# Kernel optimization log

Measured on AMD Instinct MI355X. Metric: run time of the kernel, lower is better.

The kernel has to match this reference:

```python
import jax, jax.numpy as jnp
import numpy as np

# (in_dim, out_dim) for fc1..fc14, hard-coded in the torch module
DIMS = [(12,12),(12,11),(11,10),(10,9),(9,8),(8,7),(7,6),(6,7),(7,8),(8,9),(9,10),(10,11),(11,12),(12,2)]
BATCH = 2_000_000


def setup_inputs() -> dict:
    key = jax.random.key(0)
    keys = jax.random.split(key, 2 * len(DIMS) + 1)
    inp = {"x": jax.random.normal(keys[0], (BATCH, 12), dtype=jnp.float32)}
    for i, (din, dout) in enumerate(DIMS):
        s = 1.0 / np.sqrt(din)  # torch nn.Linear default init range
        inp[f"w{i+1}"] = jax.random.uniform(keys[2*i+1], (dout, din), jnp.float32, -s, s)
        inp[f"b{i+1}"] = jax.random.uniform(keys[2*i+2], (dout,), jnp.float32, -s, s)
    return inp


def _forward(x, Ws, Bs):
    lin = lambda h, i: h @ Ws[i].T + Bs[i]
    # encoder half: fc1..fc6 with ReLU, saving identities 1..6
    ids = []
    h = x
    for i in range(6):
        h = jax.nn.relu(lin(h, i))
        ids.append(h)
    # bottleneck fc7
    h = jax.nn.relu(lin(h, 6))
    # decoder half: fc8..fc13, each adds the matching identity before ReLU
    # fc8 (+id6), fc9 (+id5), ..., fc13 (+id1)
    for i in range(7, 13):
        h = jax.nn.relu(lin(h, i) + ids[12 - i])
    # fc14 + softmax over class dim
    return jax.nn.softmax(lin(h, 13), axis=1)


def reference(x, w1, b1, w2, b2, w3, b3, w4, b4, w5, b5, w6, b6, w7, b7,
              w8, b8, w9, b9, w10, b10, w11, b11, w12, b12, w13, b13, w14, b14):
    Ws = [w1, w2, w3, w4, w5, w6, w7, w8, w9, w10, w11, w12, w13, w14]
    Bs = [b1, b2, b3, b4, b5, b6, b7, b8, b9, b10, b11, b12, b13, b14]
    return _forward(x, Ws, Bs)
```

## Files before the change

kernel.cpp:

```cpp
#include <hip/hip_runtime.h>
#include <math.h>

#define DEV __device__ __forceinline__

template <int DIN, int DOUT>
DEV void lin(const float* __restrict__ w, const float* __restrict__ b,
             const float* in, float* out) {
#pragma unroll
    for (int o = 0; o < DOUT; ++o) out[o] = b[o];
#pragma unroll
    for (int k = 0; k < DIN; ++k) {
        float xk = in[k];
#pragma unroll
        for (int o = 0; o < DOUT; ++o)
            out[o] = __builtin_fmaf(xk, w[o * DIN + k], out[o]);
    }
}

template <int DIN, int DOUT>
DEV void lin_skip(const float* __restrict__ w, const float* __restrict__ b,
                  const float* in, const float* skip, float* out) {
#pragma unroll
    for (int o = 0; o < DOUT; ++o) out[o] = b[o] + skip[o];
#pragma unroll
    for (int k = 0; k < DIN; ++k) {
        float xk = in[k];
#pragma unroll
        for (int o = 0; o < DOUT; ++o)
            out[o] = __builtin_fmaf(xk, w[o * DIN + k], out[o]);
    }
}

template <int N>
DEV void relu_ip(float* v) {
#pragma unroll
    for (int k = 0; k < N; ++k) v[k] = fmaxf(v[k], 0.0f);
}

__global__ void __launch_bounds__(256, 4)
csnet14_kernel(const float* __restrict__ x,
               const float* __restrict__ w1,  const float* __restrict__ b1,
               const float* __restrict__ w2,  const float* __restrict__ b2,
               const float* __restrict__ w3,  const float* __restrict__ b3,
               const float* __restrict__ w4,  const float* __restrict__ b4,
               const float* __restrict__ w5,  const float* __restrict__ b5,
               const float* __restrict__ w6,  const float* __restrict__ b6,
               const float* __restrict__ w7,  const float* __restrict__ b7,
               const float* __restrict__ w8,  const float* __restrict__ b8,
               const float* __restrict__ w9,  const float* __restrict__ b9,
               const float* __restrict__ w10, const float* __restrict__ b10,
               const float* __restrict__ w11, const float* __restrict__ b11,
               const float* __restrict__ w12, const float* __restrict__ b12,
               const float* __restrict__ w13, const float* __restrict__ b13,
               const float* __restrict__ w14, const float* __restrict__ b14,
               float* __restrict__ out, int n) {
    int t = blockIdx.x * blockDim.x + threadIdx.x;
    if (t >= n) return;

    const float4* xr = reinterpret_cast<const float4*>(x + (size_t)t * 12);
    float4 a0 = xr[0], a1 = xr[1], a2 = xr[2];
    float h0[12] = {a0.x, a0.y, a0.z, a0.w, a1.x, a1.y, a1.z, a1.w,
                    a2.x, a2.y, a2.z, a2.w};

    float id1[12]; lin<12, 12>(w1, b1, h0,  id1); relu_ip<12>(id1);
    float id2[11]; lin<12, 11>(w2, b2, id1, id2); relu_ip<11>(id2);
    float id3[10]; lin<11, 10>(w3, b3, id2, id3); relu_ip<10>(id3);
    float id4[9];  lin<10,  9>(w4, b4, id3, id4); relu_ip<9>(id4);
    float id5[8];  lin< 9,  8>(w5, b5, id4, id5); relu_ip<8>(id5);
    float id6[7];  lin< 8,  7>(w6, b6, id5, id6); relu_ip<7>(id6);

    float t7[6];   lin< 7,  6>(w7, b7, id6, t7);  relu_ip<6>(t7);

    float t8[7];   lin_skip< 6,  7>(w8,  b8,  t7,  id6, t8);  relu_ip<7>(t8);
    float t9[8];   lin_skip< 7,  8>(w9,  b9,  t8,  id5, t9);  relu_ip<8>(t9);
    float t10[9];  lin_skip< 8,  9>(w10, b10, t9,  id4, t10); relu_ip<9>(t10);
    float t11[10]; lin_skip< 9, 10>(w11, b11, t10, id3, t11); relu_ip<10>(t11);
    float t12[11]; lin_skip<10, 11>(w12, b12, t11, id2, t12); relu_ip<11>(t12);
    float t13[12]; lin_skip<11, 12>(w13, b13, t12, id1, t13); relu_ip<12>(t13);

    float l[2];    lin<12,  2>(w14, b14, t13, l);
    float m  = fmaxf(l[0], l[1]);
    float e0 = __expf(l[0] - m);
    float e1 = __expf(l[1] - m);
    float inv = __builtin_amdgcn_rcpf(e0 + e1);

    float2 o;
    o.x = e0 * inv;
    o.y = e1 * inv;
    reinterpret_cast<float2*>(out)[t] = o;
}

extern "C" void kernel_launch(void* const* d_in, const int* in_sizes, int n_in,
                              void* d_out, int out_size, void* d_ws, size_t ws_size,
                              hipStream_t stream) {
    const float* x   = (const float*)d_in[0];
    const float* w1  = (const float*)d_in[1];  const float* b1  = (const float*)d_in[2];
    const float* w2  = (const float*)d_in[3];  const float* b2  = (const float*)d_in[4];
    const float* w3  = (const float*)d_in[5];  const float* b3  = (const float*)d_in[6];
    const float* w4  = (const float*)d_in[7];  const float* b4  = (const float*)d_in[8];
    const float* w5  = (const float*)d_in[9];  const float* b5  = (const float*)d_in[10];
    const float* w6  = (const float*)d_in[11]; const float* b6  = (const float*)d_in[12];
    const float* w7  = (const float*)d_in[13]; const float* b7  = (const float*)d_in[14];
    const float* w8  = (const float*)d_in[15]; const float* b8  = (const float*)d_in[16];
    const float* w9  = (const float*)d_in[17]; const float* b9  = (const float*)d_in[18];
    const float* w10 = (const float*)d_in[19]; const float* b10 = (const float*)d_in[20];
    const float* w11 = (const float*)d_in[21]; const float* b11 = (const float*)d_in[22];
    const float* w12 = (const float*)d_in[23]; const float* b12 = (const float*)d_in[24];
    const float* w13 = (const float*)d_in[25]; const float* b13 = (const float*)d_in[26];
    const float* w14 = (const float*)d_in[27]; const float* b14 = (const float*)d_in[28];
    float* out = (float*)d_out;

    const int n = in_sizes[0] / 12;
    dim3 block(256);
    dim3 grid((n + 255) / 256);
    csnet14_kernel<<<grid, block, 0, stream>>>(
        x, w1, b1, w2, b2, w3, b3, w4, b4, w5, b5, w6, b6, w7, b7,
        w8, b8, w9, b9, w10, b10, w11, b11, w12, b12, w13, b13, w14, b14,
        out, n);
}
```

Measured before the change: 242.6 us.

## Use packed fp16 dot2 for MLP layers with repacked weights in device global

Adds a small repack kernel that converts all weights to packed half2 pairs and biases to a single device-global array. The main kernel then quantizes activations to fp16 pairs and computes each layer with v_dot2 (fp16 inputs, fp32 accumulate), which halves the FMA instruction count. The weights now come from one fixed global symbol, so they can be loaded as uniform scalar loads. This costs an extra launch per call and adds fp16 rounding error on inputs, activations and weights, which may exceed tolerance.

```diff
diff --git a/kernel.cpp b/kernel.cpp
--- a/kernel.cpp
+++ b/kernel.cpp
@@ -3,82 +3,190 @@
 
 #define DEV __device__ __forceinline__
 
-template <int DIN, int DOUT>
-DEV void lin(const float* __restrict__ w, const float* __restrict__ b,
-             const float* in, float* out) {
-#pragma unroll
-    for (int o = 0; o < DOUT; ++o) out[o] = b[o];
-#pragma unroll
-    for (int k = 0; k < DIN; ++k) {
-        float xk = in[k];
-#pragma unroll
-        for (int o = 0; o < DOUT; ++o)
-            out[o] = __builtin_fmaf(xk, w[o * DIN + k], out[o]);
-    }
-}
-
-template <int DIN, int DOUT>
-DEV void lin_skip(const float* __restrict__ w, const float* __restrict__ b,
-                  const float* in, const float* skip, float* out) {
-#pragma unroll
-    for (int o = 0; o < DOUT; ++o) out[o] = b[o] + skip[o];
-#pragma unroll
-    for (int k = 0; k < DIN; ++k) {
-        float xk = in[k];
-#pragma unroll
-        for (int o = 0; o < DOUT; ++o)
-            out[o] = __builtin_fmaf(xk, w[o * DIN + k], out[o]);
+
+typedef _Float16 h2 __attribute__((ext_vector_type(2)));
+
+DEV unsigned h2u(h2 h) { union { h2 h; unsigned u; } c; c.h = h; return c.u; }
+DEV h2 u2h(unsigned u) { union { unsigned u; h2 h; } c; c.u = u; return c.h; }
+
+#define UW1  0
+#define UW2  72
+#define UW3  140
+#define UW4  200
+#define UW5  248
+#define UW6  288
+#define UW7  316
+#define UW8  340
+#define UW9  364
+#define UW10 396
+#define UW11 432
+#define UW12 484
+#define UW13 540
+#define UW14 612
+#define OB1  624
+#define OB2  636
+#define OB3  648
+#define OB4  660
+#define OB5  672
+#define OB6  680
+#define OB7  688
+#define OB8  696
+#define OB9  704
+#define OB10 712
+#define OB11 724
+#define OB12 736
+#define OB13 748
+#define OB14 760
+#define WTOT 764
+
+__device__ __attribute__((aligned(16))) unsigned Wq[WTOT];
+
+__global__ void repack_kernel(
+    const float* w1,  const float* b1,  const float* w2,  const float* b2,
+    const float* w3,  const float* b3,  const float* w4,  const float* b4,
+    const float* w5,  const float* b5,  const float* w6,  const float* b6,
+    const float* w7,  const float* b7,  const float* w8,  const float* b8,
+    const float* w9,  const float* b9,  const float* w10, const float* b10,
+    const float* w11, const float* b11, const float* w12, const float* b12,
+    const float* w13, const float* b13, const float* w14, const float* b14) {
+    struct L { const float* w; const float* b; int din, dout, uw, ob; };
+    const L ls[14] = {
+        {w1,  b1,  12, 12, UW1,  OB1},  {w2,  b2,  12, 11, UW2,  OB2},
+        {w3,  b3,  11, 10, UW3,  OB3},  {w4,  b4,  10,  9, UW4,  OB4},
+        {w5,  b5,   9,  8, UW5,  OB5},  {w6,  b6,   8,  7, UW6,  OB6},
+        {w7,  b7,   7,  6, UW7,  OB7},  {w8,  b8,   6,  7, UW8,  OB8},
+        {w9,  b9,   7,  8, UW9,  OB9},  {w10, b10,  8,  9, UW10, OB10},
+        {w11, b11,  9, 10, UW11, OB11}, {w12, b12, 10, 11, UW12, OB12},
+        {w13, b13, 11, 12, UW13, OB13}, {w14, b14, 12,  2, UW14, OB14}};
+    const int tid = threadIdx.x;
+    for (int s = 0; s < 14; ++s) {
+        const L& l = ls[s];
+        const int kp = (l.din + 1) / 2;
+        for (int i = tid; i < l.dout * kp; i += 256) {
+            int o = i / kp, p = i % kp;
+            float a = l.w[o * l.din + 2 * p];
+            float c = (2 * p + 1 < l.din) ? l.w[o * l.din + 2 * p + 1] : 0.0f;
+            h2 h; h.x = (_Float16)a; h.y = (_Float16)c;
+            Wq[l.uw + i] = h2u(h);
+        }
+        for (int i = tid; i < l.dout; i += 256)
+            Wq[l.ob + i] = __float_as_uint(l.b[i]);
+    }
+}
+
+template <int DIN, int DOUT, int UW, int OB>
+DEV void lind(const h2* a, float* acc) {
+    constexpr int KP = (DIN + 1) / 2;
+    const unsigned* __restrict__ wq =
+        (const unsigned*)__builtin_assume_aligned(&Wq[UW], 16);
+#pragma unroll
+    for (int ot = 0; ot < DOUT; ot += 4) {
+        constexpr int KPc = KP;
+        const int oe = (ot + 4 < DOUT) ? (ot + 4) : DOUT;
+        unsigned wt[24];
+#pragma unroll
+        for (int i = 0; i < 24; ++i)
+            if (i < (oe - ot) * KPc) wt[i] = wq[ot * KPc + i];
+#pragma unroll
+        for (int o = ot; o < oe; ++o) acc[o] = __uint_as_float(Wq[OB + o]);
+#pragma unroll
+        for (int p = 0; p < KPc; ++p) {
+            h2 ak = a[p];
+#pragma unroll
+            for (int o = ot; o < oe; ++o)
+                acc[o] = __builtin_amdgcn_fdot2(
+                    ak, u2h(wt[(o - ot) * KPc + p]), acc[o], false);
+        }
+    }
+}
+
+template <int DIN, int DOUT, int UW, int OB>
+DEV void lind_skip(const h2* a, const h2* skip, float* acc) {
+    constexpr int KP = (DIN + 1) / 2;
+    const unsigned* __restrict__ wq =
+        (const unsigned*)__builtin_assume_aligned(&Wq[UW], 16);
+#pragma unroll
+    for (int ot = 0; ot < DOUT; ot += 4) {
+        constexpr int KPc = KP;
+        const int oe = (ot + 4 < DOUT) ? (ot + 4) : DOUT;
+        unsigned wt[24];
+#pragma unroll
+        for (int i = 0; i < 24; ++i)
+            if (i < (oe - ot) * KPc) wt[i] = wq[ot * KPc + i];
+#pragma unroll
+        for (int o = ot; o < oe; ++o) {
+            float sv = (o & 1) ? (float)skip[o >> 1].y : (float)skip[o >> 1].x;
+            acc[o] = __uint_as_float(Wq[OB + o]) + sv;
+        }
+#pragma unroll
+        for (int p = 0; p < KPc; ++p) {
+            h2 ak = a[p];
+#pragma unroll
+            for (int o = ot; o < oe; ++o)
+                acc[o] = __builtin_amdgcn_fdot2(
+                    ak, u2h(wt[(o - ot) * KPc + p]), acc[o], false);
+        }
     }
 }
 
 template <int N>
-DEV void relu_ip(float* v) {
-#pragma unroll
-    for (int k = 0; k < N; ++k) v[k] = fmaxf(v[k], 0.0f);
+DEV void relu_pack(const float* acc, h2* p) {
+    constexpr int NP = (N + 1) / 2;
+#pragma unroll
+    for (int i = 0; i < NP; ++i) {
+        float a0 = fmaxf(acc[2 * i], 0.0f);
+        float a1 = (2 * i + 1 < N) ? fmaxf(acc[2 * i + 1], 0.0f) : 0.0f;
+        h2 h; h.x = (_Float16)a0; h.y = (_Float16)a1;
+        p[i] = h;
+    }
 }
 
 __global__ void __launch_bounds__(256, 4)
-csnet14_kernel(const float* __restrict__ x,
-               const float* __restrict__ w1,  const float* __restrict__ b1,
-               const float* __restrict__ w2,  const float* __restrict__ b2,
-               const float* __restrict__ w3,  const float* __restrict__ b3,
-               const float* __restrict__ w4,  const float* __restrict__ b4,
-               const float* __restrict__ w5,  const float* __restrict__ b5,
-               const float* __restrict__ w6,  const float* __restrict__ b6,
-               const float* __restrict__ w7,  const float* __restrict__ b7,
-               const float* __restrict__ w8,  const float* __restrict__ b8,
-               const float* __restrict__ w9,  const float* __restrict__ b9,
-               const float* __restrict__ w10, const float* __restrict__ b10,
-               const float* __restrict__ w11, const float* __restrict__ b11,
-               const float* __restrict__ w12, const float* __restrict__ b12,
-               const float* __restrict__ w13, const float* __restrict__ b13,
-               const float* __restrict__ w14, const float* __restrict__ b14,
-               float* __restrict__ out, int n) {
+csnet14_kernel(const float* __restrict__ x, float* __restrict__ out, int n) {
     int t = blockIdx.x * blockDim.x + threadIdx.x;
     if (t >= n) return;
 
     const float4* xr = reinterpret_cast<const float4*>(x + (size_t)t * 12);
-    float4 a0 = xr[0], a1 = xr[1], a2 = xr[2];
-    float h0[12] = {a0.x, a0.y, a0.z, a0.w, a1.x, a1.y, a1.z, a1.w,
-                    a2.x, a2.y, a2.z, a2.w};
-
-    float id1[12]; lin<12, 12>(w1, b1, h0,  id1); relu_ip<12>(id1);
-    float id2[11]; lin<12, 11>(w2, b2, id1, id2); relu_ip<11>(id2);
-    float id3[10]; lin<11, 10>(w3, b3, id2, id3); relu_ip<10>(id3);
-    float id4[9];  lin<10,  9>(w4, b4, id3, id4); relu_ip<9>(id4);
-    float id5[8];  lin< 9,  8>(w5, b5, id4, id5); relu_ip<8>(id5);
-    float id6[7];  lin< 8,  7>(w6, b6, id5, id6); relu_ip<7>(id6);
-
-    float t7[6];   lin< 7,  6>(w7, b7, id6, t7);  relu_ip<6>(t7);
-
-    float t8[7];   lin_skip< 6,  7>(w8,  b8,  t7,  id6, t8);  relu_ip<7>(t8);
-    float t9[8];   lin_skip< 7,  8>(w9,  b9,  t8,  id5, t9);  relu_ip<8>(t9);
-    float t10[9];  lin_skip< 8,  9>(w10, b10, t9,  id4, t10); relu_ip<9>(t10);
-    float t11[10]; lin_skip< 9, 10>(w11, b11, t10, id3, t11); relu_ip<10>(t11);
-    float t12[11]; lin_skip<10, 11>(w12, b12, t11, id2, t12); relu_ip<11>(t12);
-    float t13[12]; lin_skip<11, 12>(w13, b13, t12, id1, t13); relu_ip<12>(t13);
-
-    float l[2];    lin<12,  2>(w14, b14, t13, l);
+    float4 v0 = xr[0], v1 = xr[1], v2 = xr[2];
+    float xin[12] = {v0.x, v0.y, v0.z, v0.w, v1.x, v1.y, v1.z, v1.w,
+                     v2.x, v2.y, v2.z, v2.w};
+    h2 xp[6];
+#pragma unroll
+    for (int i = 0; i < 6; ++i) {
+        h2 h; h.x = (_Float16)xin[2 * i]; h.y = (_Float16)xin[2 * i + 1];
+        xp[i] = h;
+    }
+
+    float a1[12]; lind<12, 12, UW1, OB1>(xp, a1);
+    h2 p1[6];  relu_pack<12>(a1, p1);
+    float a2[11]; lind<12, 11, UW2, OB2>(p1, a2);
+    h2 p2[6];  relu_pack<11>(a2, p2);
+    float a3[10]; lind<11, 10, UW3, OB3>(p2, a3);
+    h2 p3[5];  relu_pack<10>(a3, p3);
+    float a4[9];  lind<10,  9, UW4, OB4>(p3, a4);
+    h2 p4[5];  relu_pack<9>(a4, p4);
+    float a5[8];  lind< 9,  8, UW5, OB5>(p4, a5);
+    h2 p5[4];  relu_pack<8>(a5, p5);
+    float a6[7];  lind< 8,  7, UW6, OB6>(p5, a6);
+    h2 p6[4];  relu_pack<7>(a6, p6);
+
+    float a7[6];  lind< 7,  6, UW7, OB7>(p6, a7);
+    h2 q7[3];  relu_pack<6>(a7, q7);
+
+    float a8[7];  lind_skip< 6,  7, UW8,  OB8 >(q7,  p6, a8);
+    h2 q8[4];  relu_pack<7>(a8, q8);
+    float a9[8];  lind_skip< 7,  8, UW9,  OB9 >(q8,  p5, a9);
+    h2 q9[4];  relu_pack<8>(a9, q9);
+    float a10[9]; lind_skip< 8,  9, UW10, OB10>(q9,  p4, a10);
+    h2 q10[5]; relu_pack<9>(a10, q10);
+    float a11[10]; lind_skip< 9, 10, UW11, OB11>(q10, p3, a11);
+    h2 q11[5]; relu_pack<10>(a11, q11);
+    float a12[11]; lind_skip<10, 11, UW12, OB12>(q11, p2, a12);
+    h2 q12[6]; relu_pack<11>(a12, q12);
+    float a13[12]; lind_skip<11, 12, UW13, OB13>(q12, p1, a13);
+    h2 q13[6]; relu_pack<12>(a13, q13);
+
+    float l[2];   lind<12,  2, UW14, OB14>(q13, l);
     float m  = fmaxf(l[0], l[1]);
     float e0 = __expf(l[0] - m);
     float e1 = __expf(l[1] - m);
@@ -111,10 +219,12 @@
     float* out = (float*)d_out;
 
     const int n = in_sizes[0] / 12;
+
+    repack_kernel<<<1, 256, 0, stream>>>(
+        w1, b1, w2, b2, w3, b3, w4, b4, w5, b5, w6, b6, w7, b7,
+        w8, b8, w9, b9, w10, b10, w11, b11, w12, b12, w13, b13, w14, b14);
+
     dim3 block(256);
     dim3 grid((n + 255) / 256);
-    csnet14_kernel<<<grid, block, 0, stream>>>(
-        x, w1, b1, w2, b2, w3, b3, w4, b4, w5, b5, w6, b6, w7, b7,
-        w8, b8, w9, b9, w10, b10, w11, b11, w12, b12, w13, b13, w14, b14,
-        out, n);
-}
+    csnet14_kernel<<<grid, block, 0, stream>>>(x, out, n);
+}
```

Measured after the change: 242.0 us. About the same (-0.3%).

## Run MLP layers on fp16 MFMA with bias folded into padded weight fragments

Applied to the files above, without the earlier changes.

Replaces the per-thread scalar FP32 FMA chain with a 32x32x16 fp16 MFMA per layer, one wave handling 32 rows. A repack kernel converts the weights to fp16 A-fragments with the bias folded in through a constant-one input column. Activations are packed to half2, ReLU and the skip add run in fp16, and lanes swap halves with a shuffle to form the next B operand. This cuts the scalar ALU work of the FP32 path, but adds an extra kernel launch and per-layer shuffles, and fp16 rounding puts accuracy at risk.

```diff
diff --git a/kernel.cpp b/kernel.cpp
--- a/kernel.cpp
+++ b/kernel.cpp
@@ -3,91 +3,153 @@
 
 #define DEV __device__ __forceinline__
 
-template <int DIN, int DOUT>
-DEV void lin(const float* __restrict__ w, const float* __restrict__ b,
-             const float* in, float* out) {
-#pragma unroll
-    for (int o = 0; o < DOUT; ++o) out[o] = b[o];
-#pragma unroll
-    for (int k = 0; k < DIN; ++k) {
-        float xk = in[k];
-#pragma unroll
-        for (int o = 0; o < DOUT; ++o)
-            out[o] = __builtin_fmaf(xk, w[o * DIN + k], out[o]);
-    }
+
+typedef _Float16 h2 __attribute__((ext_vector_type(2)));
+typedef _Float16 half8 __attribute__((ext_vector_type(8)));
+typedef float floatx16 __attribute__((ext_vector_type(16)));
+
+DEV unsigned h2u(h2 h) { union { h2 h; unsigned u; } c; c.h = h; return c.u; }
+DEV h2 u2h(unsigned u) { union { unsigned u; h2 h; } c; c.u = u; return c.h; }
+DEV unsigned pkh(float a, float b) {
+    h2 r; r.x = (_Float16)a; r.y = (_Float16)b; return h2u(r);
 }
 
-template <int DIN, int DOUT>
-DEV void lin_skip(const float* __restrict__ w, const float* __restrict__ b,
-                  const float* in, const float* skip, float* out) {
-#pragma unroll
-    for (int o = 0; o < DOUT; ++o) out[o] = b[o] + skip[o];
-#pragma unroll
-    for (int k = 0; k < DIN; ++k) {
-        float xk = in[k];
-#pragma unroll
-        for (int o = 0; o < DOUT; ++o)
-            out[o] = __builtin_fmaf(xk, w[o * DIN + k], out[o]);
+union H8U { half8 v; unsigned u[4]; uint4 q; };
+DEV half8 mkB(unsigned b0, unsigned b1, unsigned b2, unsigned b3) {
+    H8U h; h.u[0] = b0; h.u[1] = b1; h.u[2] = b2; h.u[3] = b3; return h.v;
+}
+DEV half8 a2h(uint4 a) { H8U h; h.q = a; return h.v; }
+
+__device__ __attribute__((aligned(16))) unsigned Afrag[14 * 64 * 4];
+
+__global__ void repack_kernel(
+    const float* w1,  const float* b1,  const float* w2,  const float* b2,
+    const float* w3,  const float* b3,  const float* w4,  const float* b4,
+    const float* w5,  const float* b5,  const float* w6,  const float* b6,
+    const float* w7,  const float* b7,  const float* w8,  const float* b8,
+    const float* w9,  const float* b9,  const float* w10, const float* b10,
+    const float* w11, const float* b11, const float* w12, const float* b12,
+    const float* w13, const float* b13, const float* w14, const float* b14) {
+    struct L { const float* w; const float* b; int din, dout; };
+    const L ls[14] = {
+        {w1, b1, 12, 12}, {w2, b2, 12, 11}, {w3, b3, 11, 10}, {w4, b4, 10, 9},
+        {w5, b5, 9, 8},   {w6, b6, 8, 7},   {w7, b7, 7, 6},   {w8, b8, 6, 7},
+        {w9, b9, 7, 8},   {w10, b10, 8, 9}, {w11, b11, 9, 10},
+        {w12, b12, 10, 11}, {w13, b13, 11, 12}, {w14, b14, 12, 2}};
+    const L& l = ls[blockIdx.x];
+    const int lane = threadIdx.x;
+    const int o = lane & 31, g = lane >> 5;
+    unsigned r[4];
+    for (int q = 0; q < 4; ++q) {
+        float v[2];
+        for (int s = 0; s < 2; ++s) {
+            int k = g * 8 + 2 * q + s;
+            float val = 0.0f;
+            if (o < l.dout) {
+                if (k < l.din)       val = l.w[o * l.din + k];
+                else if (k == 15)    val = l.b[o];
+            }
+            v[s] = val;
+        }
+        r[q] = pkh(v[0], v[1]);
     }
+    *reinterpret_cast<uint4*>(&Afrag[(blockIdx.x * 64 + lane) * 4]) =
+        make_uint4(r[0], r[1], r[2], r[3]);
 }
 
-template <int N>
-DEV void relu_ip(float* v) {
-#pragma unroll
-    for (int k = 0; k < N; ++k) v[k] = fmaxf(v[k], 0.0f);
+template <bool SKIP, bool SAVE>
+DEV half8 step(const floatx16 C, const unsigned* skip, unsigned* save, bool hi) {
+    unsigned p0 = pkh(C[0], C[1]);
+    unsigned p1 = pkh(C[2], C[3]);
+    unsigned p2 = pkh(C[4], C[5]);
+    unsigned p3 = pkh(C[6], C[7]);
+    if (SKIP) {
+        p0 = h2u(u2h(p0) + u2h(skip[0]));
+        p1 = h2u(u2h(p1) + u2h(skip[1]));
+        p2 = h2u(u2h(p2) + u2h(skip[2]));
+        p3 = h2u(u2h(p3) + u2h(skip[3]));
+    }
+    h2 z; z.x = (_Float16)0.0f; z.y = (_Float16)0.0f;
+    p0 = h2u(__builtin_elementwise_max(u2h(p0), z));
+    p1 = h2u(__builtin_elementwise_max(u2h(p1), z));
+    p2 = h2u(__builtin_elementwise_max(u2h(p2), z));
+    p3 = h2u(__builtin_elementwise_max(u2h(p3), z));
+    if (SAVE) { save[0] = p0; save[1] = p1; save[2] = p2; save[3] = p3; }
+    unsigned s0 = __shfl_xor((int)p0, 32);
+    unsigned s1 = __shfl_xor((int)p1, 32);
+    unsigned s2 = __shfl_xor((int)p2, 32);
+    unsigned s3 = __shfl_xor((int)p3, 32);
+    unsigned B0 = hi ? s2 : p0;
+    unsigned B1 = hi ? s3 : p1;
+    unsigned B2 = hi ? p2 : s0;
+    unsigned B3 = hi ? (p3 | 0x3C000000u) : s1;
+    return mkB(B0, B1, B2, B3);
 }
 
-__global__ void __launch_bounds__(256, 4)
-csnet14_kernel(const float* __restrict__ x,
-               const float* __restrict__ w1,  const float* __restrict__ b1,
-               const float* __restrict__ w2,  const float* __restrict__ b2,
-               const float* __restrict__ w3,  const float* __restrict__ b3,
-               const float* __restrict__ w4,  const float* __restrict__ b4,
-               const float* __restrict__ w5,  const float* __restrict__ b5,
-               const float* __restrict__ w6,  const float* __restrict__ b6,
-               const float* __restrict__ w7,  const float* __restrict__ b7,
-               const float* __restrict__ w8,  const float* __restrict__ b8,
-               const float* __restrict__ w9,  const float* __restrict__ b9,
-               const float* __restrict__ w10, const float* __restrict__ b10,
-               const float* __restrict__ w11, const float* __restrict__ b11,
-               const float* __restrict__ w12, const float* __restrict__ b12,
-               const float* __restrict__ w13, const float* __restrict__ b13,
-               const float* __restrict__ w14, const float* __restrict__ b14,
-               float* __restrict__ out, int n) {
-    int t = blockIdx.x * blockDim.x + threadIdx.x;
-    if (t >= n) return;
+#define MFMA(aw, B, Z) \
+    __builtin_amdgcn_mfma_f32_32x32x16_f16(a2h(aw), B, Z, 0, 0, 0)
 
-    const float4* xr = reinterpret_cast<const float4*>(x + (size_t)t * 12);
-    float4 a0 = xr[0], a1 = xr[1], a2 = xr[2];
-    float h0[12] = {a0.x, a0.y, a0.z, a0.w, a1.x, a1.y, a1.z, a1.w,
-                    a2.x, a2.y, a2.z, a2.w};
+__global__ void __launch_bounds__(256)
+csnet14_kernel(const float* __restrict__ x, float* __restrict__ out, int n) {
+    const int tid  = threadIdx.x;
+    const int lane = tid & 63;
+    const int wv   = tid >> 6;
+    const int b    = lane & 31;
+    const bool hi  = lane >= 32;
+    const int wrow = (blockIdx.x * 4 + wv) * 32;
+    if (wrow >= n) return;
+    const int row = wrow + b;
 
-    float id1[12]; lin<12, 12>(w1, b1, h0,  id1); relu_ip<12>(id1);
-    float id2[11]; lin<12, 11>(w2, b2, id1, id2); relu_ip<11>(id2);
-    float id3[10]; lin<11, 10>(w3, b3, id2, id3); relu_ip<10>(id3);
-    float id4[9];  lin<10,  9>(w4, b4, id3, id4); relu_ip<9>(id4);
-    float id5[8];  lin< 9,  8>(w5, b5, id4, id5); relu_ip<8>(id5);
-    float id6[7];  lin< 8,  7>(w6, b6, id5, id6); relu_ip<7>(id6);
+    const float4* xp = reinterpret_cast<const float4*>(x + (size_t)row * 12);
+    float4 A0 = xp[hi ? 2 : 0];
+    float4 A1 = xp[1];
+    unsigned i0 = pkh(A0.x, A0.y), i1 = pkh(A0.z, A0.w);
+    unsigned i2 = hi ? 0u          : pkh(A1.x, A1.y);
+    unsigned i3 = hi ? 0x3C000000u : pkh(A1.z, A1.w);
+    half8 B = mkB(i0, i1, i2, i3);
 
-    float t7[6];   lin< 7,  6>(w7, b7, id6, t7);  relu_ip<6>(t7);
+    floatx16 Z;
+#pragma unroll
+    for (int i = 0; i < 16; ++i) Z[i] = 0.0f;
 
-    float t8[7];   lin_skip< 6,  7>(w8,  b8,  t7,  id6, t8);  relu_ip<7>(t8);
-    float t9[8];   lin_skip< 7,  8>(w9,  b9,  t8,  id5, t9);  relu_ip<8>(t9);
-    float t10[9];  lin_skip< 8,  9>(w10, b10, t9,  id4, t10); relu_ip<9>(t10);
-    float t11[10]; lin_skip< 9, 10>(w11, b11, t10, id3, t11); relu_ip<10>(t11);
-    float t12[11]; lin_skip<10, 11>(w12, b12, t11, id2, t12); relu_ip<11>(t12);
-    float t13[12]; lin_skip<11, 12>(w13, b13, t12, id1, t13); relu_ip<12>(t13);
+    const uint4* Af = reinterpret_cast<const uint4*>(Afrag);
+    uint4 aw0  = Af[0 * 64 + lane],  aw1  = Af[1 * 64 + lane];
+    uint4 aw2  = Af[2 * 64 + lane],  aw3  = Af[3 * 64 + lane];
+    uint4 aw4  = Af[4 * 64 + lane],  aw5  = Af[5 * 64 + lane];
+    uint4 aw6  = Af[6 * 64 + lane],  aw7  = Af[7 * 64 + lane];
+    uint4 aw8  = Af[8 * 64 + lane],  aw9  = Af[9 * 64 + lane];
+    uint4 aw10 = Af[10 * 64 + lane], aw11 = Af[11 * 64 + lane];
+    uint4 aw12 = Af[12 * 64 + lane], aw13 = Af[13 * 64 + lane];
 
-    float l[2];    lin<12,  2>(w14, b14, t13, l);
-    float m  = fmaxf(l[0], l[1]);
-    float e0 = __expf(l[0] - m);
-    float e1 = __expf(l[1] - m);
-    float inv = __builtin_amdgcn_rcpf(e0 + e1);
+    unsigned id1[4], id2[4], id3[4], id4[4], id5[4], id6[4];
+    floatx16 C;
 
-    float2 o;
-    o.x = e0 * inv;
-    o.y = e1 * inv;
-    reinterpret_cast<float2*>(out)[t] = o;
+    C = MFMA(aw0, B, Z); B = step<false, true >(C, nullptr, id1, hi);
+    C = MFMA(aw1, B, Z); B = step<false, true >(C, nullptr, id2, hi);
+    C = MFMA(aw2, B, Z); B = step<false, true >(C, nullptr, id3, hi);
+    C = MFMA(aw3, B, Z); B = step<false, true >(C, nullptr, id4, hi);
+    C = MFMA(aw4, B, Z); B = step<false, true >(C, nullptr, id5, hi);
+    C = MFMA(aw5, B, Z); B = step<false, true >(C, nullptr, id6, hi);
+    C = MFMA(aw6, B, Z); B = step<false, false>(C, nullptr, nullptr, hi);
+    C = MFMA(aw7,  B, Z); B = step<true, false>(C, id6, nullptr, hi);
+    C = MFMA(aw8,  B, Z); B = step<true, false>(C, id5, nullptr, hi);
+    C = MFMA(aw9,  B, Z); B = step<true, false>(C, id4, nullptr, hi);
+    C = MFMA(aw10, B, Z); B = step<true, false>(C, id3, nullptr, hi);
+    C = MFMA(aw11, B, Z); B = step<true, false>(C, id2, nullptr, hi);
+    C = MFMA(aw12, B, Z); B = step<true, false>(C, id1, nullptr, hi);
+    C = MFMA(aw13, B, Z);
+
+    if (!hi) {
+        float l0 = C[0], l1 = C[1];
+        float m  = fmaxf(l0, l1);
+        float e0 = __expf(l0 - m);
+        float e1 = __expf(l1 - m);
+        float inv = __builtin_amdgcn_rcpf(e0 + e1);
+        float2 o2;
+        o2.x = e0 * inv;
+        o2.y = e1 * inv;
+        reinterpret_cast<float2*>(out)[row] = o2;
+    }
 }
 
 extern "C" void kernel_launch(void* const* d_in, const int* in_sizes, int n_in,
@@ -111,10 +173,12 @@
     float* out = (float*)d_out;
 
     const int n = in_sizes[0] / 12;
+
+    repack_kernel<<<14, 64, 0, stream>>>(
+        w1, b1, w2, b2, w3, b3, w4, b4, w5, b5, w6, b6, w7, b7,
+        w8, b8, w9, b9, w10, b10, w11, b11, w12, b12, w13, b13, w14, b14);
+
     dim3 block(256);
-    dim3 grid((n + 255) / 256);
-    csnet14_kernel<<<grid, block, 0, stream>>>(
-        x, w1, b1, w2, b2, w3, b3, w4, b4, w5, b5, w6, b6, w7, b7,
-        w8, b8, w9, b9, w10, b10, w11, b11, w12, b12, w13, b13, w14, b14,
-        out, n);
+    dim3 grid((n + 127) / 128);
+    csnet14_kernel<<<grid, block, 0, stream>>>(x, out, n);
 }
```

New measurement: 218.1 us. -10.1%, faster.
